# Kernel optimization log

Measured on AMD Instinct MI355X. Metric: run time of the kernel, lower is better.

## Reference

```python
import jax, jax.numpy as jnp
import numpy as np

FEATURE_DIM = 512
HIDDEN_DIM = 512
N_HEADS = 8
HEAD_DIM = HIDDEN_DIM // N_HEADS
MAX_LEN = 5000
GAMMA = 0.5  # gaussian relative-position bias width
LN_EPS = 1e-5


def make_pe(d_model, max_len):
    # sinusoidal positional encoding buffer, as in PositionalEncoding.__init__
    pos = jnp.arange(max_len, dtype=jnp.float32)[:, None]
    div = jnp.exp(jnp.arange(0, d_model, 2, dtype=jnp.float32) * (-np.log(10000.0) / d_model))
    ang = pos * div  # [max_len, d_model/2]
    pe = jnp.zeros((max_len, d_model), dtype=jnp.float32)
    pe = pe.at[:, 0::2].set(jnp.sin(ang)).at[:, 1::2].set(jnp.cos(ang))
    return pe


def setup_inputs() -> dict:
    key = jax.random.key(0)
    k_x, k_q, k_k, k_v = jax.random.split(key, 4)
    xavier = np.sqrt(6.0 / (FEATURE_DIM + HEAD_DIM))  # xavier_uniform over last two dims
    return {
        "data_window": jax.random.normal(k_x, (1, 2048, FEATURE_DIM), dtype=jnp.float32),
        "W_query": jax.random.uniform(k_q, (N_HEADS, FEATURE_DIM, HEAD_DIM), jnp.float32, -xavier, xavier),
        "W_key": jax.random.uniform(k_k, (N_HEADS, FEATURE_DIM, HEAD_DIM), jnp.float32, -xavier, xavier),
        "W_value": jax.random.uniform(k_v, (N_HEADS, FEATURE_DIM, HEAD_DIM), jnp.float32, -xavier, xavier),
        "ln_gamma": jnp.ones((FEATURE_DIM,), dtype=jnp.float32),
        "ln_beta": jnp.zeros((FEATURE_DIM,), dtype=jnp.float32),
    }


def reference(data_window, W_query, W_key, W_value, ln_gamma, ln_beta):
    B, S, F = data_window.shape
    temperature = 1.0

    # LayerNorm over feature dim
    mu = jnp.mean(data_window, axis=-1, keepdims=True)
    var = jnp.mean(jnp.square(data_window - mu), axis=-1, keepdims=True)
    x = (data_window - mu) * jax.lax.rsqrt(var + LN_EPS) * ln_gamma + ln_beta

    # positional encoding, exactly as original: x + pe[:x.shape[0]] (requires B==1)
    pe = make_pe(FEATURE_DIM, MAX_LEN)
    x = x + pe[:B]  # [B,F] broadcasts over [B,S,F] only because B==1

    # per-head QKV projections, vectorized over heads
    Q = jnp.einsum('bsf,hfd->bhsd', x, W_query)
    K = jnp.einsum('bsf,hfd->bhsd', x, W_key)
    V = jnp.einsum('bsf,hfd->bhsd', x, W_value)

    scores = jnp.einsum('bhsd,bhtd->bhst', Q, K) / np.sqrt(HEAD_DIM)

    # gaussian relative-position bias: scale(=1) * exp(-gamma * (i-j)^2)
    p = jnp.arange(S, dtype=jnp.float32)
    rel = p[:, None] - p[None, :]
    bias = jnp.exp(-GAMMA * jnp.square(rel))  # [S,S]
    scores = (scores + bias[None, None]) / temperature
    # dropout on scores is identity in eval mode

    attn = jax.nn.softmax(scores, axis=-1)  # [B,H,S,S]
    head_out = jnp.einsum('bhst,bhtd->bhsd', attn, V)

    # concat heads along feature dim: [B,S,H*D]
    multi_head_output = head_out.transpose(0, 2, 1, 3).reshape(B, S, N_HEADS * HEAD_DIM)
    mean_weights = jnp.mean(attn, axis=1)  # [B,S,S]
    return multi_head_output, mean_weights
```

## Files before the change

### kernel.cpp

```cpp
#include <hip/hip_runtime.h>
#include <hip/hip_bf16.h>
#include <math.h>

#define S_LEN 2048
#define FDIM  512
#define NH    8
#define HD    64
#define MH_ELEMS (S_LEN * FDIM)
#define MEAN_ELEMS (S_LEN * S_LEN)
#define LOG2E 1.44269504f
#define LN2   0.69314718f

typedef _Float16 half_t;
typedef _Float16 half2v __attribute__((ext_vector_type(2)));
typedef _Float16 half4v __attribute__((ext_vector_type(4)));
typedef _Float16 half8v __attribute__((ext_vector_type(8)));
typedef float    float4v __attribute__((ext_vector_type(4)));
typedef int      int4v   __attribute__((ext_vector_type(4)));

#define MFMA16(a, b, c) __builtin_amdgcn_mfma_f32_16x16x32_f16((a), (b), (c), 0, 0, 0)

static __device__ __forceinline__ float fast_exp2(float x) {
    return __builtin_amdgcn_exp2f(x);
}

__global__ __launch_bounds__(256) void prep_kernel(const float* __restrict__ x,
                                                   const float* __restrict__ gamma,
                                                   const float* __restrict__ beta,
                                                   const float* __restrict__ Wq,
                                                   const float* __restrict__ Wk,
                                                   const float* __restrict__ Wv,
                                                   half_t* __restrict__ xo,
                                                   half_t* __restrict__ WT) {
    const int tid = threadIdx.x;
    if (blockIdx.x < 2048) {
        const int row = blockIdx.x;
        const float2 v = ((const float2*)(x + (size_t)row * FDIM))[tid];
        float s = v.x + v.y;
        float q = v.x * v.x + v.y * v.y;
        #pragma unroll
        for (int off = 1; off < 64; off <<= 1) {
            s += __shfl_xor(s, off, 64);
            q += __shfl_xor(q, off, 64);
        }
        __shared__ float red[8];
        const int wave = tid >> 6;
        if ((tid & 63) == 0) { red[wave] = s; red[4 + wave] = q; }
        __syncthreads();
        s = red[0] + red[1] + red[2] + red[3];
        q = red[4] + red[5] + red[6] + red[7];
        const float mu  = s * (1.0f / FDIM);
        const float var = q * (1.0f / FDIM) - mu * mu;
        const float rstd = rsqrtf(var + 1e-5f);
        const int f0 = tid * 2, f1 = tid * 2 + 1;
        const float o0 = (v.x - mu) * rstd * gamma[f0] + beta[f0];
        const float o1 = (v.y - mu) * rstd * gamma[f1] + beta[f1] + 1.0f;
        half2v o; o.x = (half_t)o0; o.y = (half_t)o1;
        ((half2v*)(xo + (size_t)row * FDIM))[tid] = o;
    } else {
        const int idx = blockIdx.x - 2048;
        const int k0 = (idx & 7) * 64;
        const int h  = (idx >> 3) & 7;
        const int z  = idx >> 6;
        const float* W = ((z == 0) ? Wq : (z == 1) ? Wk : Wv) + (size_t)h * FDIM * HD;
        __shared__ float Ls[64][65];
        {
            const int kk = tid >> 2, dg = (tid & 3) * 16;
            #pragma unroll
            for (int j = 0; j < 4; ++j) {
                const float4 w = *(const float4*)(W + (size_t)(k0 + kk) * HD + dg + j * 4);
                Ls[kk][dg + j * 4 + 0] = w.x; Ls[kk][dg + j * 4 + 1] = w.y;
                Ls[kk][dg + j * 4 + 2] = w.z; Ls[kk][dg + j * 4 + 3] = w.w;
            }
        }
        __syncthreads();
        {
            const int d = tid >> 2, kg = (tid & 3) * 16;
            half8v t0, t1;
            #pragma unroll
            for (int j = 0; j < 8; ++j) t0[j] = (half_t)Ls[kg + j][d];
            #pragma unroll
            for (int j = 0; j < 8; ++j) t1[j] = (half_t)Ls[kg + 8 + j][d];
            half_t* dst = WT + ((size_t)(z * NH + h) * HD + d) * FDIM + k0 + kg;
            *(half8v*)dst = t0;
            *(half8v*)(dst + 8) = t1;
        }
    }
}

__global__ __launch_bounds__(256) void qkv_kernel(const half_t* __restrict__ xh,
                                                  const half_t* __restrict__ WT,
                                                  half_t* __restrict__ Qo,
                                                  half_t* __restrict__ Ko,
                                                  half_t* __restrict__ VTo) {
    const int ms0 = blockIdx.x * 128;
    const int h   = blockIdx.y, z = blockIdx.z;
    const half_t* Wt = WT + (size_t)(z * NH + h) * HD * FDIM;

    const int tid = threadIdx.x;
    const int wv = tid >> 6, lane = tid & 63;
    const int lo = lane & 15, qq = lane >> 4;

    float4v acc[2][4];
    #pragma unroll
    for (int rg = 0; rg < 2; ++rg)
        #pragma unroll
        for (int cg = 0; cg < 4; ++cg) acc[rg][cg] = (float4v){0.f, 0.f, 0.f, 0.f};

    const half_t* ar[2];
    ar[0] = xh + (size_t)(ms0 + wv * 32 + lo) * FDIM + qq * 8;
    ar[1] = ar[0] + 16 * FDIM;
    const half_t* wrow[4];
    #pragma unroll
    for (int cg = 0; cg < 4; ++cg) wrow[cg] = Wt + (size_t)(cg * 16 + lo) * FDIM + qq * 8;

    half8v a_c[2][2], b_c[4][2];
    #pragma unroll
    for (int rg = 0; rg < 2; ++rg) { a_c[rg][0] = *(const half8v*)(ar[rg]); a_c[rg][1] = *(const half8v*)(ar[rg] + 32); }
    #pragma unroll
    for (int cg = 0; cg < 4; ++cg) { b_c[cg][0] = *(const half8v*)(wrow[cg]); b_c[cg][1] = *(const half8v*)(wrow[cg] + 32); }

    for (int k0 = 0; k0 < FDIM; k0 += 64) {
        const int kn0 = (k0 + 64 < FDIM) ? k0 + 64 : 0;
        const int kn1 = (k0 + 96 < FDIM) ? k0 + 96 : 0;
        half8v a_n[2][2], b_n[4][2];
        #pragma unroll
        for (int rg = 0; rg < 2; ++rg) { a_n[rg][0] = *(const half8v*)(ar[rg] + kn0); a_n[rg][1] = *(const half8v*)(ar[rg] + kn1); }
        #pragma unroll
        for (int cg = 0; cg < 4; ++cg) { b_n[cg][0] = *(const half8v*)(wrow[cg] + kn0); b_n[cg][1] = *(const half8v*)(wrow[cg] + kn1); }
        #pragma unroll
        for (int kh = 0; kh < 2; ++kh)
            #pragma unroll
            for (int rg = 0; rg < 2; ++rg)
                #pragma unroll
                for (int cg = 0; cg < 4; ++cg)
                    acc[rg][cg] = MFMA16(a_c[rg][kh], b_c[cg][kh], acc[rg][cg]);
        #pragma unroll
        for (int rg = 0; rg < 2; ++rg) { a_c[rg][0] = a_n[rg][0]; a_c[rg][1] = a_n[rg][1]; }
        #pragma unroll
        for (int cg = 0; cg < 4; ++cg) { b_c[cg][0] = b_n[cg][0]; b_c[cg][1] = b_n[cg][1]; }
    }

    if (z < 2) {
        half_t* Co = ((z == 0) ? Qo : Ko) + (size_t)h * S_LEN * HD;
        #pragma unroll
        for (int rg = 0; rg < 2; ++rg)
            #pragma unroll
            for (int cg = 0; cg < 4; ++cg)
                #pragma unroll
                for (int r = 0; r < 4; ++r)
                    Co[(size_t)(ms0 + wv * 32 + rg * 16 + qq * 4 + r) * HD + cg * 16 + lo] =
                        (half_t)acc[rg][cg][r];
    } else {
        __shared__ float Ls[128][65];
        #pragma unroll
        for (int rg = 0; rg < 2; ++rg)
            #pragma unroll
            for (int cg = 0; cg < 4; ++cg)
                #pragma unroll
                for (int r = 0; r < 4; ++r)
                    Ls[wv * 32 + rg * 16 + qq * 4 + r][cg * 16 + lo] = acc[rg][cg][r];
        __syncthreads();
        const int d = tid & 63, sg = tid >> 6;
        half_t* dst = VTo + (size_t)(h * HD + d) * S_LEN + ms0 + sg * 32;
        #pragma unroll
        for (int c = 0; c < 4; ++c) {
            half8v t;
            #pragma unroll
            for (int j = 0; j < 8; ++j) t[j] = (half_t)Ls[sg * 32 + c * 8 + j][d];
            *(half8v*)(dst + c * 8) = t;
        }
    }
}

__global__ __launch_bounds__(256) void attn2_kernel(const half_t* __restrict__ Qw,
                                                    const half_t* __restrict__ Kw,
                                                    const half_t* __restrict__ VT,
                                                    half_t* __restrict__ Op,
                                                    float* __restrict__ mp,
                                                    float* __restrict__ lp) {
    const int s0 = blockIdx.x * 32;
    const int h  = blockIdx.y;
    const int z  = blockIdx.z;
    const half_t* Qh = Qw + (size_t)h * S_LEN * HD;
    const half_t* Kh = Kw + (size_t)h * S_LEN * HD;
    const half_t* Vt = VT + (size_t)h * (size_t)HD * S_LEN;

    __shared__ float Osh[4][32][65];
    __shared__ float lsh[4][32];
    __shared__ float msh[4][32];

    const int tid = threadIdx.x;
    const int wv = tid >> 6, lane = tid & 63;
    const int lo = lane & 15, qq = lane >> 4;
    const int tb = z * 1024 + wv * 256;

    const half8v qA0 = *(const half8v*)(Qh + (size_t)(s0 + lo) * HD + qq * 8);
    const half8v qA1 = *(const half8v*)(Qh + (size_t)(s0 + lo) * HD + 32 + qq * 8);
    const half8v qB0 = *(const half8v*)(Qh + (size_t)(s0 + 16 + lo) * HD + qq * 8);
    const half8v qB1 = *(const half8v*)(Qh + (size_t)(s0 + 16 + lo) * HD + 32 + qq * 8);

    float4v accA[4], accB[4];
    #pragma unroll
    for (int dt = 0; dt < 4; ++dt) {
        accA[dt] = (float4v){0.f, 0.f, 0.f, 0.f};
        accB[dt] = (float4v){0.f, 0.f, 0.f, 0.f};
    }
    float mA = 0.f, mB = 0.f, lA = 0.f, lB = 0.f;

    const int srcLow  = lo + ((qq & 1) * 2) * 16;
    const int srcHigh = srcLow + 16;
    const bool sel1 = (qq >> 1) != 0;

    half8v kc[4];
    {
        const half_t* kp0 = Kh + (size_t)(tb + lo) * HD;
        const half_t* kp1 = Kh + (size_t)(tb + 16 + lo) * HD;
        kc[0] = *(const half8v*)(kp0 + qq * 8);
        kc[1] = *(const half8v*)(kp0 + 32 + qq * 8);
        kc[2] = *(const half8v*)(kp1 + qq * 8);
        kc[3] = *(const half8v*)(kp1 + 32 + qq * 8);
    }

    for (int ps = 0; ps < 8; ++ps) {
        const int Tg  = tb + ps * 32;
        const int Tgn = tb + ((ps < 7) ? ps + 1 : ps) * 32;
        half8v kn[4], vc[4];
        {
            const half_t* kp0 = Kh + (size_t)(Tgn + lo) * HD;
            const half_t* kp1 = Kh + (size_t)(Tgn + 16 + lo) * HD;
            kn[0] = *(const half8v*)(kp0 + qq * 8);
            kn[1] = *(const half8v*)(kp0 + 32 + qq * 8);
            kn[2] = *(const half8v*)(kp1 + qq * 8);
            kn[3] = *(const half8v*)(kp1 + 32 + qq * 8);
            #pragma unroll
            for (int dt = 0; dt < 4; ++dt)
                vc[dt] = *(const half8v*)(Vt + (size_t)(dt * 16 + lo) * S_LEN + Tg + qq * 8);
        }
        float4v c0A = (float4v){0.f, 0.f, 0.f, 0.f};
        c0A = MFMA16(kc[0], qA0, c0A); c0A = MFMA16(kc[1], qA1, c0A);
        float4v c1A = (float4v){0.f, 0.f, 0.f, 0.f};
        c1A = MFMA16(kc[2], qA0, c1A); c1A = MFMA16(kc[3], qA1, c1A);
        float4v c0B = (float4v){0.f, 0.f, 0.f, 0.f};
        c0B = MFMA16(kc[0], qB0, c0B); c0B = MFMA16(kc[1], qB1, c0B);
        float4v c1B = (float4v){0.f, 0.f, 0.f, 0.f};
        c1B = MFMA16(kc[2], qB0, c1B); c1B = MFMA16(kc[3], qB1, c1B);

        const int dd0 = s0 - Tg;
        const bool nA0 = (dd0 > -40) && (dd0 < 40);
        const bool nA1 = (dd0 - 16 > -40) && (dd0 - 16 < 40);
        const bool nB0 = (dd0 + 16 > -40) && (dd0 + 16 < 40);
        const bool nB1 = nA0;
        float S0A[4], S1A[4], S0B[4], S1B[4];
        #pragma unroll
        for (int r = 0; r < 4; ++r) {
            const int t0 = Tg + qq * 4 + r, t1 = t0 + 16;
            float sa0 = c0A[r] * 0.125f;
            if (nA0) { const float d = (float)(s0 + lo - t0); sa0 += __expf(-0.5f * d * d); }
            float sa1 = c1A[r] * 0.125f;
            if (nA1) { const float d = (float)(s0 + lo - t1); sa1 += __expf(-0.5f * d * d); }
            float sb0 = c0B[r] * 0.125f;
            if (nB0) { const float d = (float)(s0 + 16 + lo - t0); sb0 += __expf(-0.5f * d * d); }
            float sb1 = c1B[r] * 0.125f;
            if (nB1) { const float d = (float)(s0 + 16 + lo - t1); sb1 += __expf(-0.5f * d * d); }
            S0A[r] = sa0 * LOG2E; S1A[r] = sa1 * LOG2E;
            S0B[r] = sb0 * LOG2E; S1B[r] = sb1 * LOG2E;
        }
        float smA = fmaxf(fmaxf(fmaxf(S0A[0], S0A[1]), fmaxf(S0A[2], S0A[3])),
                          fmaxf(fmaxf(S1A[0], S1A[1]), fmaxf(S1A[2], S1A[3])));
        float smB = fmaxf(fmaxf(fmaxf(S0B[0], S0B[1]), fmaxf(S0B[2], S0B[3])),
                          fmaxf(fmaxf(S1B[0], S1B[1]), fmaxf(S1B[2], S1B[3])));
        smA = fmaxf(smA, __shfl_xor(smA, 16, 64));
        smA = fmaxf(smA, __shfl_xor(smA, 32, 64));
        smB = fmaxf(smB, __shfl_xor(smB, 16, 64));
        smB = fmaxf(smB, __shfl_xor(smB, 32, 64));
        const float gmax = fmaxf(smA - mA, smB - mB);
        if (!__all(gmax <= 5.77f)) {
            const float mnA = fmaxf(mA, smA), mnB = fmaxf(mB, smB);
            const float alA = fast_exp2(mA - mnA), alB = fast_exp2(mB - mnB);
            mA = mnA; mB = mnB;
            lA *= alA; lB *= alB;
            #pragma unroll
            for (int dt = 0; dt < 4; ++dt)
                #pragma unroll
                for (int i = 0; i < 4; ++i) { accA[dt][i] *= alA; accB[dt][i] *= alB; }
        }
        float E0A[4], E1A[4], E0B[4], E1B[4];
        float lsA = 0.f, lsB = 0.f;
        #pragma unroll
        for (int r = 0; r < 4; ++r) {
            E0A[r] = fast_exp2(S0A[r] - mA); E1A[r] = fast_exp2(S1A[r] - mA);
            E0B[r] = fast_exp2(S0B[r] - mB); E1B[r] = fast_exp2(S1B[r] - mB);
            lsA += E0A[r] + E1A[r];
            lsB += E0B[r] + E1B[r];
        }
        lA += lsA;
        lB += lsB;

        int pkA0, pkA1, pkA2, pkA3, pkB0, pkB1, pkB2, pkB3;
        {
            half2v p;
            p.x = (half_t)E0A[0]; p.y = (half_t)E0A[1]; pkA0 = __builtin_bit_cast(int, p);
            p.x = (half_t)E0A[2]; p.y = (half_t)E0A[3]; pkA1 = __builtin_bit_cast(int, p);
            p.x = (half_t)E1A[0]; p.y = (half_t)E1A[1]; pkA2 = __builtin_bit_cast(int, p);
            p.x = (half_t)E1A[2]; p.y = (half_t)E1A[3]; pkA3 = __builtin_bit_cast(int, p);
            p.x = (half_t)E0B[0]; p.y = (half_t)E0B[1]; pkB0 = __builtin_bit_cast(int, p);
            p.x = (half_t)E0B[2]; p.y = (half_t)E0B[3]; pkB1 = __builtin_bit_cast(int, p);
            p.x = (half_t)E1B[0]; p.y = (half_t)E1B[1]; pkB2 = __builtin_bit_cast(int, p);
            p.x = (half_t)E1B[2]; p.y = (half_t)E1B[3]; pkB3 = __builtin_bit_cast(int, p);
        }
        int4v biA, biB;
        {
            const int l0a = __shfl(pkA0, srcLow, 64),  l0b = __shfl(pkA2, srcLow, 64);
            const int l1a = __shfl(pkA1, srcLow, 64),  l1b = __shfl(pkA3, srcLow, 64);
            const int h0a = __shfl(pkA0, srcHigh, 64), h0b = __shfl(pkA2, srcHigh, 64);
            const int h1a = __shfl(pkA1, srcHigh, 64), h1b = __shfl(pkA3, srcHigh, 64);
            biA[0] = sel1 ? l0b : l0a;
            biA[1] = sel1 ? l1b : l1a;
            biA[2] = sel1 ? h0b : h0a;
            biA[3] = sel1 ? h1b : h1a;
        }
        {
            const int l0a = __shfl(pkB0, srcLow, 64),  l0b = __shfl(pkB2, srcLow, 64);
            const int l1a = __shfl(pkB1, srcLow, 64),  l1b = __shfl(pkB3, srcLow, 64);
            const int h0a = __shfl(pkB0, srcHigh, 64), h0b = __shfl(pkB2, srcHigh, 64);
            const int h1a = __shfl(pkB1, srcHigh, 64), h1b = __shfl(pkB3, srcHigh, 64);
            biB[0] = sel1 ? l0b : l0a;
            biB[1] = sel1 ? l1b : l1a;
            biB[2] = sel1 ? h0b : h0a;
            biB[3] = sel1 ? h1b : h1a;
        }
        const half8v bpA = __builtin_bit_cast(half8v, biA);
        const half8v bpB = __builtin_bit_cast(half8v, biB);
        #pragma unroll
        for (int dt = 0; dt < 4; ++dt) {
            accA[dt] = MFMA16(vc[dt], bpA, accA[dt]);
            accB[dt] = MFMA16(vc[dt], bpB, accB[dt]);
        }
        #pragma unroll
        for (int i = 0; i < 4; ++i) kc[i] = kn[i];
    }

    lA += __shfl_xor(lA, 16, 64); lA += __shfl_xor(lA, 32, 64);
    lB += __shfl_xor(lB, 16, 64); lB += __shfl_xor(lB, 32, 64);
    if (qq == 0) {
        lsh[wv][lo] = lA;      msh[wv][lo] = mA;
        lsh[wv][16 + lo] = lB; msh[wv][16 + lo] = mB;
    }
    #pragma unroll
    for (int dt = 0; dt < 4; ++dt)
        #pragma unroll
        for (int r = 0; r < 4; ++r) {
            Osh[wv][lo][dt * 16 + qq * 4 + r]      = accA[dt][r];
            Osh[wv][16 + lo][dt * 16 + qq * 4 + r] = accB[dt][r];
        }
    __syncthreads();

    #pragma unroll
    for (int p = 0; p < 2; ++p) {
        const int q = p * 16 + (tid >> 4), dg = tid & 15;
        const float m0 = msh[0][q], m1 = msh[1][q], m2 = msh[2][q], m3 = msh[3][q];
        const float M = fmaxf(fmaxf(m0, m1), fmaxf(m2, m3));
        const float f0 = fast_exp2(m0 - M), f1 = fast_exp2(m1 - M);
        const float f2 = fast_exp2(m2 - M), f3 = fast_exp2(m3 - M);
        const float L = lsh[0][q] * f0 + lsh[1][q] * f1 + lsh[2][q] * f2 + lsh[3][q] * f3;
        half4v o;
        #pragma unroll
        for (int i = 0; i < 4; ++i) {
            const float ov = Osh[0][q][dg * 4 + i] * f0 + Osh[1][q][dg * 4 + i] * f1 +
                             Osh[2][q][dg * 4 + i] * f2 + Osh[3][q][dg * 4 + i] * f3;
            o[i] = (half_t)ov;
        }
        const size_t pidx = (size_t)(z * NH + h) * S_LEN + s0 + q;
        *(half4v*)(Op + pidx * HD + dg * 4) = o;
        if (dg == 0) { mp[pidx] = M * LN2; lp[pidx] = L; }
    }
}

__global__ __launch_bounds__(256) void mean2_kernel(const half_t* __restrict__ Qw,
                                                    const half_t* __restrict__ Kw,
                                                    const half_t* __restrict__ Op,
                                                    const float* __restrict__ mp,
                                                    const float* __restrict__ lp,
                                                    float* __restrict__ out) {
    const int q0 = blockIdx.x * 32;
    const int tbase = blockIdx.y * 256;
    const int tid = threadIdx.x;

    __shared__ float lnc[NH][32];
    __shared__ float g0s[NH][32];
    __shared__ float g1s[NH][32];
    {
        const int h = tid >> 5, qi = tid & 31;
        const size_t i0 = (size_t)h * S_LEN + q0 + qi;
        const size_t i1 = (size_t)(NH + h) * S_LEN + q0 + qi;
        const float m0 = mp[i0], m1 = mp[i1];
        const float M = fmaxf(m0, m1);
        const float f0 = __expf(m0 - M), f1 = __expf(m1 - M);
        const float L = lp[i0] * f0 + lp[i1] * f1;
        const float inv = 1.0f / L;
        lnc[h][qi] = -M - __logf(L);
        g0s[h][qi] = f0 * inv;
        g1s[h][qi] = f1 * inv;
    }
    __syncthreads();

    const int wv = tid >> 6, lane = tid & 63;
    const int lo = lane & 15, qq = lane >> 4;
    const int t0 = tbase + wv * 64;

    float4v macc[2][4];
    #pragma unroll
    for (int rg = 0; rg < 2; ++rg)
        #pragma unroll
        for (int tg = 0; tg < 4; ++tg) macc[rg][tg] = (float4v){0.f, 0.f, 0.f, 0.f};

    const half_t* qp = Qw + (size_t)(q0 + lo) * HD + qq * 8;
    const half_t* kp = Kw + (size_t)(t0 + lo) * HD + qq * 8;

    #pragma unroll 2
    for (int h = 0; h < NH; ++h) {
        half8v a[2][2], b[4][2];
        #pragma unroll
        for (int rg = 0; rg < 2; ++rg) {
            a[rg][0] = *(const half8v*)(qp + (size_t)rg * 16 * HD);
            a[rg][1] = *(const half8v*)(qp + (size_t)rg * 16 * HD + 32);
        }
        #pragma unroll
        for (int tg = 0; tg < 4; ++tg) {
            b[tg][0] = *(const half8v*)(kp + (size_t)tg * 16 * HD);
            b[tg][1] = *(const half8v*)(kp + (size_t)tg * 16 * HD + 32);
        }
        float4v sacc[2][4];
        #pragma unroll
        for (int rg = 0; rg < 2; ++rg)
            #pragma unroll
            for (int tg = 0; tg < 4; ++tg) sacc[rg][tg] = (float4v){0.f, 0.f, 0.f, 0.f};
        #pragma unroll
        for (int kh = 0; kh < 2; ++kh)
            #pragma unroll
            for (int rg = 0; rg < 2; ++rg)
                #pragma unroll
                for (int tg = 0; tg < 4; ++tg)
                    sacc[rg][tg] = MFMA16(a[rg][kh], b[tg][kh], sacc[rg][tg]);

        const float4v ln0 = *(const float4v*)&lnc[h][qq * 4];
        const float4v ln1 = *(const float4v*)&lnc[h][16 + qq * 4];
        #pragma unroll
        for (int tg = 0; tg < 4; ++tg)
            #pragma unroll
            for (int r = 0; r < 4; ++r) {
                macc[0][tg][r] += __expf(fmaf(sacc[0][tg][r], 0.125f, ln0[r]));
                macc[1][tg][r] += __expf(fmaf(sacc[1][tg][r], 0.125f, ln1[r]));
            }
        qp += (size_t)S_LEN * HD;
        kp += (size_t)S_LEN * HD;
    }

    #pragma unroll
    for (int rg = 0; rg < 2; ++rg)
        #pragma unroll
        for (int tg = 0; tg < 4; ++tg) {
            const int tgl = t0 + tg * 16;
            const bool near = ((q0 + 31 - tgl) > -40) && ((q0 - (tgl + 15)) < 40);
            #pragma unroll
            for (int r = 0; r < 4; ++r) {
                const int qe = q0 + rg * 16 + qq * 4 + r;
                const int te = tgl + lo;
                float w = macc[rg][tg][r] * 0.125f;
                if (near) {
                    const float d = (float)(qe - te);
                    w *= __expf(__expf(-0.5f * d * d));
                }
                out[MH_ELEMS + (size_t)qe * S_LEN + te] = w;
            }
        }

    if (blockIdx.y == 0) {
        const int qi = tid >> 3, dg = (tid & 7) * 8;
        const int q = q0 + qi;
        #pragma unroll
        for (int h = 0; h < NH; ++h) {
            const half8v o0 = *(const half8v*)(Op + ((size_t)h * S_LEN + q) * HD + dg);
            const half8v o1 = *(const half8v*)(Op + ((size_t)(NH + h) * S_LEN + q) * HD + dg);
            const float a0 = g0s[h][qi], a1 = g1s[h][qi];
            float4 r0, r1;
            r0.x = (float)o0[0] * a0 + (float)o1[0] * a1;
            r0.y = (float)o0[1] * a0 + (float)o1[1] * a1;
            r0.z = (float)o0[2] * a0 + (float)o1[2] * a1;
            r0.w = (float)o0[3] * a0 + (float)o1[3] * a1;
            r1.x = (float)o0[4] * a0 + (float)o1[4] * a1;
            r1.y = (float)o0[5] * a0 + (float)o1[5] * a1;
            r1.z = (float)o0[6] * a0 + (float)o1[6] * a1;
            r1.w = (float)o0[7] * a0 + (float)o1[7] * a1;
            float* dst = out + (size_t)q * FDIM + h * HD + dg;
            *(float4*)dst = r0;
            *(float4*)(dst + 4) = r1;
        }
    }
}

extern "C" void kernel_launch(void* const* d_in, const int* in_sizes, int n_in,
                              void* d_out, int out_size, void* d_ws, size_t ws_size,
                              hipStream_t stream) {
    const float* x  = (const float*)d_in[0];
    const float* Wq = (const float*)d_in[1];
    const float* Wk = (const float*)d_in[2];
    const float* Wv = (const float*)d_in[3];
    const float* g  = (const float*)d_in[4];
    const float* b  = (const float*)d_in[5];
    float* out = (float*)d_out;
    char*  ws  = (char*)d_ws;

    half_t* Qh   = (half_t*)(ws);
    half_t* Kh   = (half_t*)(ws + (2ull  << 20));
    half_t* VT   = (half_t*)(ws + (4ull  << 20));
    half_t* xh   = (half_t*)(ws + (6ull  << 20));
    half_t* WT   = (half_t*)(ws + (8ull  << 20));
    half_t* Op   = (half_t*)(ws + (10ull << 20));
    float*  mp   = (float*) (ws + (14ull << 20));
    float*  lp   = (float*) (ws + (14ull << 20) + (128ull << 10));

    prep_kernel<<<2240, 256, 0, stream>>>(x, g, b, Wq, Wk, Wv, xh, WT);
    qkv_kernel<<<dim3(16, 8, 3), 256, 0, stream>>>(xh, WT, Qh, Kh, VT);
    attn2_kernel<<<dim3(64, 8, 2), 256, 0, stream>>>(Qh, Kh, VT, Op, mp, lp);
    mean2_kernel<<<dim3(64, 8), 256, 0, stream>>>(Qh, Kh, Op, mp, lp, out);
}
```

Before: 161.3 us.

## Software-pipeline QK^T scores ahead of softmax/PV and halve mean kernel query tile

In the attention kernel, the QK^T MFMAs and bias/scale for the next key tile are now computed while the current tile's softmax and PV MFMAs run, and K is prefetched two tiles ahead. The conditional lazy rescale is replaced by an unconditional rescale every step. Scale and exp constants are folded into base-2 so the kernels can use native exp2. The mean-weights kernel now handles 16 queries per block instead of 32 and launches twice as many blocks. The gains come from better latency hiding and more parallelism, at the cost of higher register pressure and an extra rescale multiply on every iteration.

```diff
diff --git a/kernel.cpp b/kernel.cpp
--- a/kernel.cpp
+++ b/kernel.cpp
@@ -10,6 +10,8 @@
 #define MEAN_ELEMS (S_LEN * S_LEN)
 #define LOG2E 1.44269504f
 #define LN2   0.69314718f
+#define QK_SCALE_L2 0.18033688f
+#define NEG_HALF_L2 0.72134752f
 
 typedef _Float16 half_t;
 typedef _Float16 half2v __attribute__((ext_vector_type(2)));
@@ -173,12 +175,12 @@
     }
 }
 
-__global__ __launch_bounds__(256) void attn2_kernel(const half_t* __restrict__ Qw,
-                                                    const half_t* __restrict__ Kw,
-                                                    const half_t* __restrict__ VT,
-                                                    half_t* __restrict__ Op,
-                                                    float* __restrict__ mp,
-                                                    float* __restrict__ lp) {
+__global__ __launch_bounds__(256, 4) void attn2_kernel(const half_t* __restrict__ Qw,
+                                                       const half_t* __restrict__ Kw,
+                                                       const half_t* __restrict__ VT,
+                                                       half_t* __restrict__ Op,
+                                                       float* __restrict__ mp,
+                                                       float* __restrict__ lp) {
     const int s0 = blockIdx.x * 32;
     const int h  = blockIdx.y;
     const int z  = blockIdx.z;
@@ -212,60 +214,82 @@
     const int srcHigh = srcLow + 16;
     const bool sel1 = (qq >> 1) != 0;
 
+    float S0A[4], S1A[4], S0B[4], S1B[4];
     half8v kc[4];
+
     {
+        half8v k0[4];
         const half_t* kp0 = Kh + (size_t)(tb + lo) * HD;
         const half_t* kp1 = Kh + (size_t)(tb + 16 + lo) * HD;
-        kc[0] = *(const half8v*)(kp0 + qq * 8);
-        kc[1] = *(const half8v*)(kp0 + 32 + qq * 8);
-        kc[2] = *(const half8v*)(kp1 + qq * 8);
-        kc[3] = *(const half8v*)(kp1 + 32 + qq * 8);
-    }
-
-    for (int ps = 0; ps < 8; ++ps) {
-        const int Tg  = tb + ps * 32;
-        const int Tgn = tb + ((ps < 7) ? ps + 1 : ps) * 32;
-        half8v kn[4], vc[4];
-        {
-            const half_t* kp0 = Kh + (size_t)(Tgn + lo) * HD;
-            const half_t* kp1 = Kh + (size_t)(Tgn + 16 + lo) * HD;
-            kn[0] = *(const half8v*)(kp0 + qq * 8);
-            kn[1] = *(const half8v*)(kp0 + 32 + qq * 8);
-            kn[2] = *(const half8v*)(kp1 + qq * 8);
-            kn[3] = *(const half8v*)(kp1 + 32 + qq * 8);
-            #pragma unroll
-            for (int dt = 0; dt < 4; ++dt)
-                vc[dt] = *(const half8v*)(Vt + (size_t)(dt * 16 + lo) * S_LEN + Tg + qq * 8);
-        }
+        k0[0] = *(const half8v*)(kp0 + qq * 8);
+        k0[1] = *(const half8v*)(kp0 + 32 + qq * 8);
+        k0[2] = *(const half8v*)(kp1 + qq * 8);
+        k0[3] = *(const half8v*)(kp1 + 32 + qq * 8);
+        const half_t* kp2 = Kh + (size_t)(tb + 32 + lo) * HD;
+        const half_t* kp3 = Kh + (size_t)(tb + 48 + lo) * HD;
+        kc[0] = *(const half8v*)(kp2 + qq * 8);
+        kc[1] = *(const half8v*)(kp2 + 32 + qq * 8);
+        kc[2] = *(const half8v*)(kp3 + qq * 8);
+        kc[3] = *(const half8v*)(kp3 + 32 + qq * 8);
+
         float4v c0A = (float4v){0.f, 0.f, 0.f, 0.f};
-        c0A = MFMA16(kc[0], qA0, c0A); c0A = MFMA16(kc[1], qA1, c0A);
+        c0A = MFMA16(k0[0], qA0, c0A); c0A = MFMA16(k0[1], qA1, c0A);
         float4v c1A = (float4v){0.f, 0.f, 0.f, 0.f};
-        c1A = MFMA16(kc[2], qA0, c1A); c1A = MFMA16(kc[3], qA1, c1A);
+        c1A = MFMA16(k0[2], qA0, c1A); c1A = MFMA16(k0[3], qA1, c1A);
         float4v c0B = (float4v){0.f, 0.f, 0.f, 0.f};
-        c0B = MFMA16(kc[0], qB0, c0B); c0B = MFMA16(kc[1], qB1, c0B);
+        c0B = MFMA16(k0[0], qB0, c0B); c0B = MFMA16(k0[1], qB1, c0B);
         float4v c1B = (float4v){0.f, 0.f, 0.f, 0.f};
-        c1B = MFMA16(kc[2], qB0, c1B); c1B = MFMA16(kc[3], qB1, c1B);
-
+        c1B = MFMA16(k0[2], qB0, c1B); c1B = MFMA16(k0[3], qB1, c1B);
+
+        const int Tg = tb;
         const int dd0 = s0 - Tg;
         const bool nA0 = (dd0 > -40) && (dd0 < 40);
         const bool nA1 = (dd0 - 16 > -40) && (dd0 - 16 < 40);
         const bool nB0 = (dd0 + 16 > -40) && (dd0 + 16 < 40);
         const bool nB1 = nA0;
-        float S0A[4], S1A[4], S0B[4], S1B[4];
         #pragma unroll
         for (int r = 0; r < 4; ++r) {
-            const int t0 = Tg + qq * 4 + r, t1 = t0 + 16;
-            float sa0 = c0A[r] * 0.125f;
-            if (nA0) { const float d = (float)(s0 + lo - t0); sa0 += __expf(-0.5f * d * d); }
-            float sa1 = c1A[r] * 0.125f;
-            if (nA1) { const float d = (float)(s0 + lo - t1); sa1 += __expf(-0.5f * d * d); }
-            float sb0 = c0B[r] * 0.125f;
-            if (nB0) { const float d = (float)(s0 + 16 + lo - t0); sb0 += __expf(-0.5f * d * d); }
-            float sb1 = c1B[r] * 0.125f;
-            if (nB1) { const float d = (float)(s0 + 16 + lo - t1); sb1 += __expf(-0.5f * d * d); }
-            S0A[r] = sa0 * LOG2E; S1A[r] = sa1 * LOG2E;
-            S0B[r] = sb0 * LOG2E; S1B[r] = sb1 * LOG2E;
-        }
+            const int t0r = Tg + qq * 4 + r, t1r = t0r + 16;
+            float sa0 = c0A[r] * QK_SCALE_L2;
+            if (nA0) { const float d = (float)(s0 + lo - t0r); sa0 += fast_exp2(-NEG_HALF_L2 * d * d) * LOG2E; }
+            float sa1 = c1A[r] * QK_SCALE_L2;
+            if (nA1) { const float d = (float)(s0 + lo - t1r); sa1 += fast_exp2(-NEG_HALF_L2 * d * d) * LOG2E; }
+            float sb0 = c0B[r] * QK_SCALE_L2;
+            if (nB0) { const float d = (float)(s0 + 16 + lo - t0r); sb0 += fast_exp2(-NEG_HALF_L2 * d * d) * LOG2E; }
+            float sb1 = c1B[r] * QK_SCALE_L2;
+            if (nB1) { const float d = (float)(s0 + 16 + lo - t1r); sb1 += fast_exp2(-NEG_HALF_L2 * d * d) * LOG2E; }
+            S0A[r] = sa0; S1A[r] = sa1; S0B[r] = sb0; S1B[r] = sb1;
+        }
+    }
+
+    for (int ps = 0; ps < 8; ++ps) {
+        const int Tg  = tb + ps * 32;
+        const int Tg2 = tb + ((ps + 2 < 8) ? ps + 2 : 7) * 32;
+        half8v kn[4], vc[4];
+        {
+            const half_t* kp0 = Kh + (size_t)(Tg2 + lo) * HD;
+            const half_t* kp1 = Kh + (size_t)(Tg2 + 16 + lo) * HD;
+            kn[0] = *(const half8v*)(kp0 + qq * 8);
+            kn[1] = *(const half8v*)(kp0 + 32 + qq * 8);
+            kn[2] = *(const half8v*)(kp1 + qq * 8);
+            kn[3] = *(const half8v*)(kp1 + 32 + qq * 8);
+            #pragma unroll
+            for (int dt = 0; dt < 4; ++dt)
+                vc[dt] = *(const half8v*)(Vt + (size_t)(dt * 16 + lo) * S_LEN + Tg + qq * 8);
+        }
+
+        float4v n0A, n1A, n0B, n1B;
+        if (ps < 7) {
+            n0A = (float4v){0.f, 0.f, 0.f, 0.f};
+            n0A = MFMA16(kc[0], qA0, n0A); n0A = MFMA16(kc[1], qA1, n0A);
+            n1A = (float4v){0.f, 0.f, 0.f, 0.f};
+            n1A = MFMA16(kc[2], qA0, n1A); n1A = MFMA16(kc[3], qA1, n1A);
+            n0B = (float4v){0.f, 0.f, 0.f, 0.f};
+            n0B = MFMA16(kc[0], qB0, n0B); n0B = MFMA16(kc[1], qB1, n0B);
+            n1B = (float4v){0.f, 0.f, 0.f, 0.f};
+            n1B = MFMA16(kc[2], qB0, n1B); n1B = MFMA16(kc[3], qB1, n1B);
+        }
+
         float smA = fmaxf(fmaxf(fmaxf(S0A[0], S0A[1]), fmaxf(S0A[2], S0A[3])),
                           fmaxf(fmaxf(S1A[0], S1A[1]), fmaxf(S1A[2], S1A[3])));
         float smB = fmaxf(fmaxf(fmaxf(S0B[0], S0B[1]), fmaxf(S0B[2], S0B[3])),
@@ -274,17 +298,9 @@
         smA = fmaxf(smA, __shfl_xor(smA, 32, 64));
         smB = fmaxf(smB, __shfl_xor(smB, 16, 64));
         smB = fmaxf(smB, __shfl_xor(smB, 32, 64));
-        const float gmax = fmaxf(smA - mA, smB - mB);
-        if (!__all(gmax <= 5.77f)) {
-            const float mnA = fmaxf(mA, smA), mnB = fmaxf(mB, smB);
-            const float alA = fast_exp2(mA - mnA), alB = fast_exp2(mB - mnB);
-            mA = mnA; mB = mnB;
-            lA *= alA; lB *= alB;
-            #pragma unroll
-            for (int dt = 0; dt < 4; ++dt)
-                #pragma unroll
-                for (int i = 0; i < 4; ++i) { accA[dt][i] *= alA; accB[dt][i] *= alB; }
-        }
+        const float mnA = fmaxf(mA, smA), mnB = fmaxf(mB, smB);
+        const float alA = fast_exp2(mA - mnA), alB = fast_exp2(mB - mnB);
+        mA = mnA; mB = mnB;
         float E0A[4], E1A[4], E0B[4], E1B[4];
         float lsA = 0.f, lsB = 0.f;
         #pragma unroll
@@ -294,8 +310,12 @@
             lsA += E0A[r] + E1A[r];
             lsB += E0B[r] + E1B[r];
         }
-        lA += lsA;
-        lB += lsB;
+        lA = lA * alA + lsA;
+        lB = lB * alB + lsB;
+        #pragma unroll
+        for (int dt = 0; dt < 4; ++dt)
+            #pragma unroll
+            for (int i = 0; i < 4; ++i) { accA[dt][i] *= alA; accB[dt][i] *= alB; }
 
         int pkA0, pkA1, pkA2, pkA3, pkB0, pkB1, pkB2, pkB3;
         {
@@ -337,6 +357,28 @@
             accA[dt] = MFMA16(vc[dt], bpA, accA[dt]);
             accB[dt] = MFMA16(vc[dt], bpB, accB[dt]);
         }
+
+        if (ps < 7) {
+            const int Tg1 = Tg + 32;
+            const int dd0 = s0 - Tg1;
+            const bool nA0 = (dd0 > -40) && (dd0 < 40);
+            const bool nA1 = (dd0 - 16 > -40) && (dd0 - 16 < 40);
+            const bool nB0 = (dd0 + 16 > -40) && (dd0 + 16 < 40);
+            const bool nB1 = nA0;
+            #pragma unroll
+            for (int r = 0; r < 4; ++r) {
+                const int t0r = Tg1 + qq * 4 + r, t1r = t0r + 16;
+                float sa0 = n0A[r] * QK_SCALE_L2;
+                if (nA0) { const float d = (float)(s0 + lo - t0r); sa0 += fast_exp2(-NEG_HALF_L2 * d * d) * LOG2E; }
+                float sa1 = n1A[r] * QK_SCALE_L2;
+                if (nA1) { const float d = (float)(s0 + lo - t1r); sa1 += fast_exp2(-NEG_HALF_L2 * d * d) * LOG2E; }
+                float sb0 = n0B[r] * QK_SCALE_L2;
+                if (nB0) { const float d = (float)(s0 + 16 + lo - t0r); sb0 += fast_exp2(-NEG_HALF_L2 * d * d) * LOG2E; }
+                float sb1 = n1B[r] * QK_SCALE_L2;
+                if (nB1) { const float d = (float)(s0 + 16 + lo - t1r); sb1 += fast_exp2(-NEG_HALF_L2 * d * d) * LOG2E; }
+                S0A[r] = sa0; S1A[r] = sa1; S0B[r] = sb0; S1B[r] = sb1;
+            }
+        }
         #pragma unroll
         for (int i = 0; i < 4; ++i) kc[i] = kn[i];
     }
@@ -383,15 +425,15 @@
                                                     const float* __restrict__ mp,
                                                     const float* __restrict__ lp,
                                                     float* __restrict__ out) {
-    const int q0 = blockIdx.x * 32;
+    const int q0 = blockIdx.x * 16;
     const int tbase = blockIdx.y * 256;
     const int tid = threadIdx.x;
 
-    __shared__ float lnc[NH][32];
-    __shared__ float g0s[NH][32];
-    __shared__ float g1s[NH][32];
-    {
-        const int h = tid >> 5, qi = tid & 31;
+    __shared__ float lnc[NH][16];
+    __shared__ float g0s[NH][16];
+    __shared__ float g1s[NH][16];
+    if (tid < 128) {
+        const int h = tid >> 4, qi = tid & 15;
         const size_t i0 = (size_t)h * S_LEN + q0 + qi;
         const size_t i1 = (size_t)(NH + h) * S_LEN + q0 + qi;
         const float m0 = mp[i0], m1 = mp[i1];
@@ -399,7 +441,7 @@
         const float f0 = __expf(m0 - M), f1 = __expf(m1 - M);
         const float L = lp[i0] * f0 + lp[i1] * f1;
         const float inv = 1.0f / L;
-        lnc[h][qi] = -M - __logf(L);
+        lnc[h][qi] = (-M - __logf(L)) * LOG2E;
         g0s[h][qi] = f0 * inv;
         g1s[h][qi] = f1 * inv;
     }
@@ -409,93 +451,73 @@
     const int lo = lane & 15, qq = lane >> 4;
     const int t0 = tbase + wv * 64;
 
-    float4v macc[2][4];
-    #pragma unroll
-    for (int rg = 0; rg < 2; ++rg)
-        #pragma unroll
-        for (int tg = 0; tg < 4; ++tg) macc[rg][tg] = (float4v){0.f, 0.f, 0.f, 0.f};
+    float4v macc[4];
+    #pragma unroll
+    for (int tg = 0; tg < 4; ++tg) macc[tg] = (float4v){0.f, 0.f, 0.f, 0.f};
 
     const half_t* qp = Qw + (size_t)(q0 + lo) * HD + qq * 8;
     const half_t* kp = Kw + (size_t)(t0 + lo) * HD + qq * 8;
 
     #pragma unroll 2
     for (int h = 0; h < NH; ++h) {
-        half8v a[2][2], b[4][2];
-        #pragma unroll
-        for (int rg = 0; rg < 2; ++rg) {
-            a[rg][0] = *(const half8v*)(qp + (size_t)rg * 16 * HD);
-            a[rg][1] = *(const half8v*)(qp + (size_t)rg * 16 * HD + 32);
-        }
+        half8v a[2], b[4][2];
+        a[0] = *(const half8v*)(qp);
+        a[1] = *(const half8v*)(qp + 32);
         #pragma unroll
         for (int tg = 0; tg < 4; ++tg) {
             b[tg][0] = *(const half8v*)(kp + (size_t)tg * 16 * HD);
             b[tg][1] = *(const half8v*)(kp + (size_t)tg * 16 * HD + 32);
         }
-        float4v sacc[2][4];
-        #pragma unroll
-        for (int rg = 0; rg < 2; ++rg)
-            #pragma unroll
-            for (int tg = 0; tg < 4; ++tg) sacc[rg][tg] = (float4v){0.f, 0.f, 0.f, 0.f};
+        float4v sacc[4];
+        #pragma unroll
+        for (int tg = 0; tg < 4; ++tg) sacc[tg] = (float4v){0.f, 0.f, 0.f, 0.f};
         #pragma unroll
         for (int kh = 0; kh < 2; ++kh)
             #pragma unroll
-            for (int rg = 0; rg < 2; ++rg)
-                #pragma unroll
-                for (int tg = 0; tg < 4; ++tg)
-                    sacc[rg][tg] = MFMA16(a[rg][kh], b[tg][kh], sacc[rg][tg]);
+            for (int tg = 0; tg < 4; ++tg)
+                sacc[tg] = MFMA16(a[kh], b[tg][kh], sacc[tg]);
 
         const float4v ln0 = *(const float4v*)&lnc[h][qq * 4];
-        const float4v ln1 = *(const float4v*)&lnc[h][16 + qq * 4];
         #pragma unroll
         for (int tg = 0; tg < 4; ++tg)
             #pragma unroll
-            for (int r = 0; r < 4; ++r) {
-                macc[0][tg][r] += __expf(fmaf(sacc[0][tg][r], 0.125f, ln0[r]));
-                macc[1][tg][r] += __expf(fmaf(sacc[1][tg][r], 0.125f, ln1[r]));
-            }
+            for (int r = 0; r < 4; ++r)
+                macc[tg][r] += fast_exp2(fmaf(sacc[tg][r], QK_SCALE_L2, ln0[r]));
         qp += (size_t)S_LEN * HD;
         kp += (size_t)S_LEN * HD;
     }
 
     #pragma unroll
-    for (int rg = 0; rg < 2; ++rg)
-        #pragma unroll
-        for (int tg = 0; tg < 4; ++tg) {
-            const int tgl = t0 + tg * 16;
-            const bool near = ((q0 + 31 - tgl) > -40) && ((q0 - (tgl + 15)) < 40);
-            #pragma unroll
-            for (int r = 0; r < 4; ++r) {
-                const int qe = q0 + rg * 16 + qq * 4 + r;
-                const int te = tgl + lo;
-                float w = macc[rg][tg][r] * 0.125f;
-                if (near) {
-                    const float d = (float)(qe - te);
-                    w *= __expf(__expf(-0.5f * d * d));
-                }
-                out[MH_ELEMS + (size_t)qe * S_LEN + te] = w;
+    for (int tg = 0; tg < 4; ++tg) {
+        const int tgl = t0 + tg * 16;
+        const bool near = ((q0 + 15 - tgl) > -40) && ((q0 - (tgl + 15)) < 40);
+        #pragma unroll
+        for (int r = 0; r < 4; ++r) {
+            const int qe = q0 + qq * 4 + r;
+            const int te = tgl + lo;
+            float w = macc[tg][r] * 0.125f;
+            if (near) {
+                const float d = (float)(qe - te);
+                w *= fast_exp2(fast_exp2(-NEG_HALF_L2 * d * d) * LOG2E);
             }
-        }
+            out[MH_ELEMS + (size_t)qe * S_LEN + te] = w;
+        }
+    }
 
     if (blockIdx.y == 0) {
-        const int qi = tid >> 3, dg = (tid & 7) * 8;
+        const int qi = tid >> 4, dl = (tid & 15) * 4;
         const int q = q0 + qi;
         #pragma unroll
         for (int h = 0; h < NH; ++h) {
-            const half8v o0 = *(const half8v*)(Op + ((size_t)h * S_LEN + q) * HD + dg);
-            const half8v o1 = *(const half8v*)(Op + ((size_t)(NH + h) * S_LEN + q) * HD + dg);
+            const half4v o0 = *(const half4v*)(Op + ((size_t)h * S_LEN + q) * HD + dl);
+            const half4v o1 = *(const half4v*)(Op + ((size_t)(NH + h) * S_LEN + q) * HD + dl);
             const float a0 = g0s[h][qi], a1 = g1s[h][qi];
-            float4 r0, r1;
+            float4 r0;
             r0.x = (float)o0[0] * a0 + (float)o1[0] * a1;
             r0.y = (float)o0[1] * a0 + (float)o1[1] * a1;
             r0.z = (float)o0[2] * a0 + (float)o1[2] * a1;
             r0.w = (float)o0[3] * a0 + (float)o1[3] * a1;
-            r1.x = (float)o0[4] * a0 + (float)o1[4] * a1;
-            r1.y = (float)o0[5] * a0 + (float)o1[5] * a1;
-            r1.z = (float)o0[6] * a0 + (float)o1[6] * a1;
-            r1.w = (float)o0[7] * a0 + (float)o1[7] * a1;
-            float* dst = out + (size_t)q * FDIM + h * HD + dg;
-            *(float4*)dst = r0;
-            *(float4*)(dst + 4) = r1;
+            *(float4*)(out + (size_t)q * FDIM + h * HD + dl) = r0;
         }
     }
 }
@@ -524,5 +546,5 @@
     prep_kernel<<<2240, 256, 0, stream>>>(x, g, b, Wq, Wk, Wv, xh, WT);
     qkv_kernel<<<dim3(16, 8, 3), 256, 0, stream>>>(xh, WT, Qh, Kh, VT);
     attn2_kernel<<<dim3(64, 8, 2), 256, 0, stream>>>(Qh, Kh, VT, Op, mp, lp);
-    mean2_kernel<<<dim3(64, 8), 256, 0, stream>>>(Qh, Kh, Op, mp, lp, out);
+    mean2_kernel<<<dim3(128, 8), 256, 0, stream>>>(Qh, Kh, Op, mp, lp, out);
 }
```

Result: slower. 209.8 us (+30.0%).
